# Performance work log

Hardware: AMD Instinct MI355X
Metric: run time of the kernel (lower is better)

Reference implementation:

```python
import jax, jax.numpy as jnp
import numpy as np

N = 10000        # nodes
E = 160000       # edges
H = 256          # hidden_dim
K = 20           # mixture components
NL = 5           # num_layers
NODE_F = 64      # node_feature_dim
NNT = 10         # num_node_types
NET = 5          # num_edge_types + 1


def setup_inputs() -> dict:
    key = jax.random.key(0)
    ks = iter(jax.random.split(key, 64))

    def nrm(shape, fan_in):
        return jax.random.normal(next(ks), shape, jnp.float32) * (1.0 / np.sqrt(fan_in))

    inp = {}
    inp["x"] = jax.random.normal(next(ks), (N, NODE_F), jnp.float32)
    inp["edge_attr"] = jax.random.normal(next(ks), (E,), jnp.float32)
    # embeddings (weights stored as [in, out])
    inp["neW"] = nrm((NODE_F, H), NODE_F); inp["neb"] = jnp.zeros((H,), jnp.float32)
    inp["eeW"] = nrm((1, H), 1);           inp["eeb"] = jnp.zeros((H,), jnp.float32)
    # per-layer message MLPs f, g (stacked over NL layers)
    inp["fW1"] = nrm((NL, 3 * H, H), 3 * H); inp["fb1"] = jnp.zeros((NL, H), jnp.float32)
    inp["fW2"] = nrm((NL, H, H), H);         inp["fb2"] = jnp.zeros((NL, H), jnp.float32)
    inp["gW1"] = nrm((NL, 3 * H, H), 3 * H); inp["gb1"] = jnp.zeros((NL, H), jnp.float32)
    inp["gW2"] = nrm((NL, H, H), H);         inp["gb2"] = jnp.zeros((NL, H), jnp.float32)
    # per-layer GRU (PyTorch layout: weight_ih [3H, 2H], weight_hh [3H, H], gate order r,z,n)
    inp["gru_wih"] = nrm((NL, 3 * H, 2 * H), 2 * H)
    inp["gru_whh"] = nrm((NL, 3 * H, H), H)
    inp["gru_bih"] = jnp.zeros((NL, 3 * H), jnp.float32)
    inp["gru_bhh"] = jnp.zeros((NL, 3 * H), jnp.float32)
    # mlp_alpha: 3H -> H -> K
    inp["aW1"] = nrm((3 * H, H), 3 * H); inp["ab1"] = jnp.zeros((H,), jnp.float32)
    inp["aW2"] = nrm((H, K), H);         inp["ab2"] = jnp.zeros((K,), jnp.float32)
    # node_pred: 2H -> H -> NNT
    inp["npW1"] = nrm((2 * H, H), 2 * H); inp["npb1"] = jnp.zeros((H,), jnp.float32)
    inp["npW2"] = nrm((H, NNT), H);       inp["npb2"] = jnp.zeros((NNT,), jnp.float32)
    # edge_pred: H -> H -> NET*K
    inp["epW1"] = nrm((H, H), H);          inp["epb1"] = jnp.zeros((H,), jnp.float32)
    inp["epW2"] = nrm((H, NET * K), H);    inp["epb2"] = jnp.zeros((NET * K,), jnp.float32)
    inp["edge_index"] = jax.random.randint(next(ks), (2, E), 0, N)
    inp["v_t"] = N - 1
    return inp


def reference(x, edge_attr, neW, neb, eeW, eeb,
              fW1, fb1, fW2, fb2, gW1, gb1, gW2, gb2,
              gru_wih, gru_whh, gru_bih, gru_bhh,
              aW1, ab1, aW2, ab2, npW1, npb1, npW2, npb2,
              epW1, epb1, epW2, epb2, edge_index, v_t):
    src = edge_index[0]  # x_j
    dst = edge_index[1]  # x_i (aggregation target)

    h_v = x @ neW + neb                       # [N, H]
    h_e = edge_attr[:, None] @ eeW + eeb      # [E, H]

    for l in range(NL):
        cat = jnp.concatenate([h_v[dst], h_v[src], h_e], axis=-1)   # [E, 3H]
        m = jax.nn.relu(cat @ fW1[l] + fb1[l]) @ fW2[l] + fb2[l]    # [E, H]
        a = jax.nn.relu(cat @ gW1[l] + gb1[l]) @ gW2[l] + gb2[l]    # [E, H]
        agg = jax.ops.segment_sum(m * a, dst, num_segments=N)       # [N, H]
        # nn.GRU over the node dimension as a sequence (unbatched input [N, 2H])
        gi = jnp.concatenate([h_v, agg], axis=-1) @ gru_wih[l].T + gru_bih[l]  # [N, 3H]
        whh, bhh = gru_whh[l], gru_bhh[l]

        def step(h, g):
            gh = whh @ h + bhh
            ir, iz, i_n = jnp.split(g, 3)
            hr, hz, hn = jnp.split(gh, 3)
            r = jax.nn.sigmoid(ir + hr)
            z = jax.nn.sigmoid(iz + hz)
            n = jnp.tanh(i_n + r * hn)
            h2 = (1.0 - z) * n + z * h
            return h2, h2

        _, h_v = jax.lax.scan(step, jnp.zeros((H,), h_v.dtype), gi)  # [N, H]

    ge = jnp.broadcast_to(jnp.mean(h_v, axis=0), h_v.shape)          # [N, H]
    np_in = jnp.concatenate([ge, h_v], axis=-1)                      # [N, 2H]
    node_pred = jax.nn.relu(np_in @ npW1 + npb1) @ npW2 + npb2       # [N, NNT]

    h_v_t = jnp.broadcast_to(h_v[v_t], h_v.shape)                    # [N, H]
    al_in = jnp.concatenate([ge, h_v_t, h_v], axis=-1)               # [N, 3H]
    alphas = jax.nn.relu(al_in @ aW1 + ab1) @ aW2 + ab2              # [N, K]
    alphas = jax.nn.softmax(jnp.sum(alphas, axis=0, keepdims=True), axis=1)  # [1, K]

    p_v = jax.nn.softmax(node_pred, axis=-1)
    log_theta = (jax.nn.relu(h_v @ epW1 + epb1) @ epW2 + epb2).reshape(N, NET, K)
    p_e = jnp.sum(alphas * jax.nn.softmax(log_theta, axis=1), axis=-1)  # [N, NET]
    return p_v, p_e
```

## Files before the change

### kernel.cpp

```cpp
#include <hip/hip_runtime.h>
#include <hip/hip_bf16.h>

#define NN 10000
#define NE 160000

typedef _Float16 half8 __attribute__((ext_vector_type(8)));
typedef _Float16 half2v __attribute__((ext_vector_type(2)));
typedef float f32x4 __attribute__((ext_vector_type(4)));

__device__ __forceinline__ f32x4 mfma_f16(half8 a, half8 b, f32x4 c){
  return __builtin_amdgcn_mfma_f32_16x16x32_f16(a, b, c, 0, 0, 0);
}

#if defined(__has_builtin)
#if __has_builtin(__builtin_amdgcn_fdot2)
#define HAS_FDOT2 1
#endif
#endif

__device__ __forceinline__ float fdot2f(half2v a, half2v b, float c){
#ifdef HAS_FDOT2
  return __builtin_amdgcn_fdot2(a, b, c, false);
#else
  return c + (float)a[0]*(float)b[0] + (float)a[1]*(float)b[1];
#endif
}

__global__ void zero_f32_kernel(float* __restrict__ p, int n){
  int i = blockIdx.x*blockDim.x + threadIdx.x;
  int st = gridDim.x*blockDim.x;
  for (; i < n; i += st) p[i] = 0.f;
}

__global__ void cast_f16_kernel(const float* __restrict__ a, _Float16* __restrict__ o, int n){
  int i = blockIdx.x*blockDim.x + threadIdx.x;
  int st = gridDim.x*blockDim.x;
  for (; i < n; i += st) o[i] = (_Float16)a[i];
}

__global__ void prep_w1t_kernel(const float* __restrict__ f, const float* __restrict__ g,
                                _Float16* __restrict__ fT, _Float16* __restrict__ gT){
  int i = blockIdx.x*256 + threadIdx.x;
  if (i >= 5*256*768) return;
  int l = i / (256*768); int r = i % (256*768);
  int c = r / 768; int k = r % 768;
  size_t s = (size_t)l*768*256 + (size_t)k*256 + c;
  fT[i] = (_Float16)f[s]; gT[i] = (_Float16)g[s];
}
__global__ void prep_w2t_kernel(const float* __restrict__ f, const float* __restrict__ g,
                                _Float16* __restrict__ fT, _Float16* __restrict__ gT){
  int i = blockIdx.x*256 + threadIdx.x;
  if (i >= 5*256*256) return;
  int l = i / (256*256); int r = i % (256*256);
  int c = r / 256; int k = r % 256;
  size_t s = (size_t)l*256*256 + (size_t)k*256 + c;
  fT[i] = (_Float16)f[s]; gT[i] = (_Float16)g[s];
}

__global__ void hist_kernel(const int* __restrict__ dst, int* __restrict__ cnt){
  int e = blockIdx.x*256 + threadIdx.x;
  if (e < NE) atomicAdd(&cnt[dst[e]], 1);
}

__global__ __launch_bounds__(1024) void scan_off_kernel(const int* __restrict__ cnt, int* __restrict__ cur){
  __shared__ int sA[1024];
  const int t = threadIdx.x;
  int run = 0;
  for (int ch = 0; ch < 10; ++ch){
    int idx = ch*1024 + t;
    int v = (idx < NN) ? cnt[idx] : 0;
    sA[t] = v;
    __syncthreads();
    for (int o = 1; o < 1024; o <<= 1){
      int add = (t >= o) ? sA[t-o] : 0;
      __syncthreads();
      sA[t] += add;
      __syncthreads();
    }
    if (idx < NN) cur[idx] = run + sA[t] - v;
    run += sA[1023];
    __syncthreads();
  }
}

__global__ void scatter_kernel(const int* __restrict__ eidx, const float* __restrict__ ea,
                               int* __restrict__ cur, int* __restrict__ srcS,
                               int* __restrict__ dstS, float* __restrict__ eaS){
  int e = blockIdx.x*256 + threadIdx.x;
  if (e < NE){
    int d = eidx[NE + e];
    int p = atomicAdd(&cur[d], 1);
    srcS[p] = eidx[e];
    dstS[p] = d;
    eaS[p]  = ea[e];
  }
}

__global__ __launch_bounds__(256) void embed_kernel(const float* __restrict__ x,
    const float* __restrict__ neW, const float* __restrict__ neb,
    float* __restrict__ hv, _Float16* __restrict__ hvf){
  __shared__ float sx[16*64];
  int rb = blockIdx.x*16, t = threadIdx.x;
  for (int i = t; i < 16*64; i += 256) sx[i] = x[(size_t)rb*64 + i];
  __syncthreads();
  float acc[16];
  float bb = neb[t];
  #pragma unroll
  for (int r = 0; r < 16; r++) acc[r] = bb;
  for (int c = 0; c < 64; c++){
    float w = neW[c*256 + t];
    #pragma unroll
    for (int r = 0; r < 16; r++) acc[r] += sx[r*64 + c]*w;
  }
  for (int r = 0; r < 16; r++){
    hv [(size_t)(rb+r)*256 + t] = acc[r];
    hvf[(size_t)(rb+r)*256 + t] = (_Float16)acc[r];
  }
}

__global__ __launch_bounds__(256, 2) void edge_mlp_kernel(
    const _Float16* __restrict__ hvf, const float* __restrict__ eaS,
    const int* __restrict__ srcS, const int* __restrict__ dstS,
    const float* __restrict__ eeW, const float* __restrict__ eeb,
    const _Float16* __restrict__ fW1T, const float* __restrict__ fb1,
    const _Float16* __restrict__ fW2T, const float* __restrict__ fb2,
    const _Float16* __restrict__ gW1T, const float* __restrict__ gb1,
    const _Float16* __restrict__ gW2T, const float* __restrict__ gb2,
    float* __restrict__ agg)
{
  extern __shared__ char smem[];
  _Float16* sHid = (_Float16*)smem;
  float* sProd = (float*)smem;
  float* sEW  = (float*)(smem + 64*264*2);
  float* sEB  = sEW + 256;
  int*   sDst = (int*)(sEB + 256);

  const int tid = threadIdx.x;
  const int wave = tid >> 6, lane = tid & 63;
  const int l15 = lane & 15, l4 = lane >> 4;
  const int eb = blockIdx.x*64;
  if (tid < 256){ sEW[tid] = eeW[tid]; sEB[tid] = eeb[tid]; }
  if (tid < 64)  sDst[tid] = dstS[eb + tid];
  int dd[4], ss[4]; float ea[4];
  #pragma unroll
  for (int rt = 0; rt < 4; rt++){
    int e = eb + rt*16 + l15;
    dd[rt] = dstS[e]; ss[rt] = srcS[e]; ea[rt] = eaS[e];
  }
  __syncthreads();
  const int colw = wave*64;
  const f32x4 zf = {0.f, 0.f, 0.f, 0.f};

  f32x4 accM[4][4], accA[4][4];
  #pragma unroll
  for (int a_ = 0; a_ < 4; a_++)
    #pragma unroll
    for (int b_ = 0; b_ < 4; b_++){ accM[a_][b_] = zf; accA[a_][b_] = zf; }

  {
    f32x4 acc[4][4];
    #pragma unroll
    for (int a_ = 0; a_ < 4; a_++)
      #pragma unroll
      for (int b_ = 0; b_ < 4; b_++) acc[a_][b_] = zf;
    #pragma unroll 1
    for (int kc = 0; kc < 24; ++kc){
      const int kk = kc*32 + l4*8;
      half8 aF[4];
      if (kc < 8){
        #pragma unroll
        for (int rt = 0; rt < 4; rt++) aF[rt] = *(const half8*)(hvf + (size_t)dd[rt]*256 + kk);
      } else if (kc < 16){
        #pragma unroll
        for (int rt = 0; rt < 4; rt++) aF[rt] = *(const half8*)(hvf + (size_t)ss[rt]*256 + (kk - 256));
      } else {
        const int q = kk - 512;
        #pragma unroll
        for (int rt = 0; rt < 4; rt++){
          half8 v;
          #pragma unroll
          for (int j = 0; j < 8; j++) v[j] = (_Float16)(ea[rt]*sEW[q+j] + sEB[q+j]);
          aF[rt] = v;
        }
      }
      half8 bF[4];
      #pragma unroll
      for (int ct = 0; ct < 4; ct++)
        bF[ct] = *(const half8*)(fW1T + (size_t)(colw + ct*16 + l15)*768 + kk);
      #pragma unroll
      for (int rt = 0; rt < 4; rt++)
        #pragma unroll
        for (int ct = 0; ct < 4; ct++)
          acc[rt][ct] = mfma_f16(aF[rt], bF[ct], acc[rt][ct]);
    }
    #pragma unroll
    for (int ct = 0; ct < 4; ct++){
      const int col = colw + ct*16 + l15;
      const float bb = fb1[col];
      #pragma unroll
      for (int rt = 0; rt < 4; rt++)
        #pragma unroll
        for (int ri = 0; ri < 4; ri++){
          int row = rt*16 + l4*4 + ri;
          sHid[row*264 + col] = (_Float16)fmaxf(acc[rt][ct][ri] + bb, 0.f);
        }
    }
    __syncthreads();
    #pragma unroll 1
    for (int kc = 0; kc < 8; ++kc){
      const int kk = kc*32 + l4*8;
      half8 aF[4], bF[4];
      #pragma unroll
      for (int rt = 0; rt < 4; rt++) aF[rt] = *(const half8*)(sHid + (rt*16 + l15)*264 + kk);
      #pragma unroll
      for (int ct = 0; ct < 4; ct++) bF[ct] = *(const half8*)(fW2T + (size_t)(colw + ct*16 + l15)*256 + kk);
      #pragma unroll
      for (int rt = 0; rt < 4; rt++)
        #pragma unroll
        for (int ct = 0; ct < 4; ct++)
          accM[rt][ct] = mfma_f16(aF[rt], bF[ct], accM[rt][ct]);
    }
    __syncthreads();
  }

  {
    f32x4 acc[4][4];
    #pragma unroll
    for (int a_ = 0; a_ < 4; a_++)
      #pragma unroll
      for (int b_ = 0; b_ < 4; b_++) acc[a_][b_] = zf;
    #pragma unroll 1
    for (int kc = 0; kc < 24; ++kc){
      const int kk = kc*32 + l4*8;
      half8 aF[4];
      if (kc < 8){
        #pragma unroll
        for (int rt = 0; rt < 4; rt++) aF[rt] = *(const half8*)(hvf + (size_t)dd[rt]*256 + kk);
      } else if (kc < 16){
        #pragma unroll
        for (int rt = 0; rt < 4; rt++) aF[rt] = *(const half8*)(hvf + (size_t)ss[rt]*256 + (kk - 256));
      } else {
        const int q = kk - 512;
        #pragma unroll
        for (int rt = 0; rt < 4; rt++){
          half8 v;
          #pragma unroll
          for (int j = 0; j < 8; j++) v[j] = (_Float16)(ea[rt]*sEW[q+j] + sEB[q+j]);
          aF[rt] = v;
        }
      }
      half8 bF[4];
      #pragma unroll
      for (int ct = 0; ct < 4; ct++)
        bF[ct] = *(const half8*)(gW1T + (size_t)(colw + ct*16 + l15)*768 + kk);
      #pragma unroll
      for (int rt = 0; rt < 4; rt++)
        #pragma unroll
        for (int ct = 0; ct < 4; ct++)
          acc[rt][ct] = mfma_f16(aF[rt], bF[ct], acc[rt][ct]);
    }
    #pragma unroll
    for (int ct = 0; ct < 4; ct++){
      const int col = colw + ct*16 + l15;
      const float bb = gb1[col];
      #pragma unroll
      for (int rt = 0; rt < 4; rt++)
        #pragma unroll
        for (int ri = 0; ri < 4; ri++){
          int row = rt*16 + l4*4 + ri;
          sHid[row*264 + col] = (_Float16)fmaxf(acc[rt][ct][ri] + bb, 0.f);
        }
    }
    __syncthreads();
    #pragma unroll 1
    for (int kc = 0; kc < 8; ++kc){
      const int kk = kc*32 + l4*8;
      half8 aF[4], bF[4];
      #pragma unroll
      for (int rt = 0; rt < 4; rt++) aF[rt] = *(const half8*)(sHid + (rt*16 + l15)*264 + kk);
      #pragma unroll
      for (int ct = 0; ct < 4; ct++) bF[ct] = *(const half8*)(gW2T + (size_t)(colw + ct*16 + l15)*256 + kk);
      #pragma unroll
      for (int rt = 0; rt < 4; rt++)
        #pragma unroll
        for (int ct = 0; ct < 4; ct++)
          accA[rt][ct] = mfma_f16(aF[rt], bF[ct], accA[rt][ct]);
    }
    __syncthreads();
  }

  int cd = sDst[0]; float ac = 0.f;
  #pragma unroll 1
  for (int hf = 0; hf < 2; ++hf){
    #pragma unroll
    for (int ct = 0; ct < 4; ct++){
      const int col = colw + ct*16 + l15;
      const float bm = fb2[col], ba = gb2[col];
      #pragma unroll
      for (int rt2 = 0; rt2 < 2; rt2++){
        const int rt = hf*2 + rt2;
        #pragma unroll
        for (int ri = 0; ri < 4; ri++){
          int row = rt2*16 + l4*4 + ri;
          sProd[row*264 + col] = (accM[rt][ct][ri] + bm)*(accA[rt][ct][ri] + ba);
        }
      }
    }
    __syncthreads();
    for (int r = 0; r < 32; ++r){
      float v = sProd[r*264 + tid];
      int dr = sDst[hf*32 + r];
      if (dr != cd){ atomicAdd(&agg[(size_t)cd*256 + tid], ac); ac = 0.f; cd = dr; }
      ac += v;
    }
    __syncthreads();
  }
  atomicAdd(&agg[(size_t)cd*256 + tid], ac);
}

#define RB_GI 157
__global__ __launch_bounds__(256, 3) void gi_mfma_kernel(
    const _Float16* __restrict__ hvf, const _Float16* __restrict__ aggf,
    const _Float16* __restrict__ wihL, const float* __restrict__ bihL,
    float* __restrict__ gi)
{
  const int tid = threadIdx.x;
  const int wave = tid >> 6, lane = tid & 63, l15 = lane & 15, l4 = lane >> 4;
  const int rblk = blockIdx.x % RB_GI;
  const int cg   = blockIdx.x / RB_GI;
  const int rb = rblk*64;
  const int colw = cg*256 + wave*64;
  int rowc[4];
  #pragma unroll
  for (int rt = 0; rt < 4; rt++){ int r = rb + rt*16 + l15; rowc[rt] = (r < NN) ? r : NN-1; }
  const f32x4 zf = {0.f, 0.f, 0.f, 0.f};
  f32x4 acc[4][4];
  #pragma unroll
  for (int a_ = 0; a_ < 4; a_++)
    #pragma unroll
    for (int b_ = 0; b_ < 4; b_++) acc[a_][b_] = zf;
  #pragma unroll 1
  for (int kc = 0; kc < 16; ++kc){
    const int kk = kc*32 + l4*8;
    half8 aF[4], bF[4];
    if (kc < 8){
      #pragma unroll
      for (int rt = 0; rt < 4; rt++) aF[rt] = *(const half8*)(hvf + (size_t)rowc[rt]*256 + kk);
    } else {
      #pragma unroll
      for (int rt = 0; rt < 4; rt++) aF[rt] = *(const half8*)(aggf + (size_t)rowc[rt]*256 + (kk - 256));
    }
    #pragma unroll
    for (int ct = 0; ct < 4; ct++)
      bF[ct] = *(const half8*)(wihL + (size_t)(colw + ct*16 + l15)*512 + kk);
    #pragma unroll
    for (int rt = 0; rt < 4; rt++)
      #pragma unroll
      for (int ct = 0; ct < 4; ct++)
        acc[rt][ct] = mfma_f16(aF[rt], bF[ct], acc[rt][ct]);
  }
  #pragma unroll
  for (int ct = 0; ct < 4; ct++){
    const int col = colw + ct*16 + l15;
    const float bb = bihL[col];
    #pragma unroll
    for (int rt = 0; rt < 4; rt++)
      #pragma unroll
      for (int ri = 0; ri < 4; ri++){
        int row = rb + rt*16 + l4*4 + ri;
        if (row < NN) gi[(size_t)row*768 + col] = acc[rt][ct][ri] + bb;
      }
  }
}

#define FOR32(M) M(0) M(1) M(2) M(3) M(4) M(5) M(6) M(7) M(8) M(9) M(10) M(11) M(12) M(13) M(14) M(15) \
                 M(16) M(17) M(18) M(19) M(20) M(21) M(22) M(23) M(24) M(25) M(26) M(27) M(28) M(29) M(30) M(31)

#define DECL_W(i) half8 w##i;

#define LD8(dst, q, i) { float4 _a = (q)[2*(i)], _b = (q)[2*(i)+1]; \
  dst[0]=(_Float16)_a.x; dst[1]=(_Float16)_a.y; dst[2]=(_Float16)_a.z; dst[3]=(_Float16)_a.w; \
  dst[4]=(_Float16)_b.x; dst[5]=(_Float16)_b.y; dst[6]=(_Float16)_b.z; dst[7]=(_Float16)_b.w; }

#define LOAD_W(i) LD8(w##i, q0, i)

#define DOT_STEP(i) { half8 hh = ph[i]; \
  a0 = fdot2f(__builtin_shufflevector(w##i, w##i, 0, 1), __builtin_shufflevector(hh, hh, 0, 1), a0); \
  a1 = fdot2f(__builtin_shufflevector(w##i, w##i, 2, 3), __builtin_shufflevector(hh, hh, 2, 3), a1); \
  a2 = fdot2f(__builtin_shufflevector(w##i, w##i, 4, 5), __builtin_shufflevector(hh, hh, 4, 5), a2); \
  a3 = fdot2f(__builtin_shufflevector(w##i, w##i, 6, 7), __builtin_shufflevector(hh, hh, 6, 7), a3); }

__global__ __launch_bounds__(768, 1) void gru_scan7(
    const float* __restrict__ whhL, const float* __restrict__ bhhL,
    const float* __restrict__ gi, float* __restrict__ hv, _Float16* __restrict__ hvf)
{
  const int t = threadIdx.x;
  FOR32(DECL_W)
  {
    const float4* q0 = (const float4*)(whhL + (size_t)t*256);
    FOR32(LOAD_W)
  }
  const float bh = bhhL[t];
  __shared__ float sGH[768];
  __shared__ __align__(16) _Float16 sH16[256];
  float h = 0.f;
  if (t < 256) sH16[t] = (_Float16)0.f;
  float gr = 0.f, gz = 0.f, gn = 0.f;
  if (t < 256){ gr = gi[t]; gz = gi[256 + t]; gn = gi[512 + t]; }
  __syncthreads();
  #pragma unroll 1
  for (int step = 0; step < NN; ++step){
    float pr = 0.f, pz = 0.f, pn = 0.f;
    if (t < 256){
      const float* g = gi + (size_t)((step + 1 < NN) ? step + 1 : step)*768;
      pr = g[t]; pz = g[256 + t]; pn = g[512 + t];
    }
    const half8* ph = (const half8*)sH16;
    float a0 = 0.f, a1 = 0.f, a2 = 0.f, a3 = 0.f;
    FOR32(DOT_STEP)
    sGH[t] = (a0 + a1) + (a2 + a3) + bh;
    __syncthreads();
    if (t < 256){
      float hr = sGH[t], hz = sGH[256 + t], hn = sGH[512 + t];
      float r = 1.f/(1.f + __expf(-(gr + hr)));
      float z = 1.f/(1.f + __expf(-(gz + hz)));
      float xx = gn + r*hn;
      xx = fminf(fmaxf(xx, -15.f), 15.f);
      float e2 = __expf(2.f*xx);
      float n = (e2 - 1.f)/(e2 + 1.f);
      h = n + z*(h - n);
      hv [(size_t)step*256 + t] = h;
      hvf[(size_t)step*256 + t] = (_Float16)h;
      sH16[t] = (_Float16)h;
      gr = pr; gz = pz; gn = pn;
    }
    __syncthreads();
  }
}

__global__ __launch_bounds__(256) void ge_sum_kernel(const float* __restrict__ hv, float* __restrict__ ge){
  int rb = blockIdx.x*40, t = threadIdx.x;
  float s = 0.f;
  for (int i = 0; i < 40; i++) s += hv[(size_t)(rb + i)*256 + t];
  atomicAdd(&ge[t], s);
}

__global__ void finalize_kernel(const float* __restrict__ ge, const float* __restrict__ hv,
                                const int* __restrict__ vt, float* __restrict__ gem, float* __restrict__ hvt){
  int t = threadIdx.x;
  gem[t] = ge[t]*(1.0f/NN);
  hvt[t] = hv[(size_t)vt[0]*256 + t];
}

__global__ __launch_bounds__(256) void base_np_kernel(const float* __restrict__ gem,
    const float* __restrict__ npW1, const float* __restrict__ npb1, float* __restrict__ bnp){
  __shared__ float sg[256];
  int t = threadIdx.x; sg[t] = gem[t]; __syncthreads();
  float a = npb1[t];
  for (int c = 0; c < 256; c++) a += sg[c]*npW1[c*256 + t];
  bnp[t] = a;
}

__global__ __launch_bounds__(256) void base_al_kernel(const float* __restrict__ gem,
    const float* __restrict__ hvt, const float* __restrict__ aW1,
    const float* __restrict__ ab1, float* __restrict__ bal){
  __shared__ float sg[256], sv[256];
  int t = threadIdx.x; sg[t] = gem[t]; sv[t] = hvt[t]; __syncthreads();
  float a = ab1[t];
  for (int c = 0; c < 256; c++) a += sg[c]*aW1[c*256 + t];
  for (int c = 0; c < 256; c++) a += sv[c]*aW1[(256 + c)*256 + t];
  bal[t] = a;
}

__global__ __launch_bounds__(256) void node_pred_kernel(const float* __restrict__ hv,
    const float* __restrict__ bnp, const float* __restrict__ npW1,
    const float* __restrict__ npW2, const float* __restrict__ npb2,
    float* __restrict__ outPV){
  __shared__ float sHv[16*256];
  __shared__ float sHid[16*257];
  __shared__ float sLg[16*10];
  int rb = blockIdx.x*16, t = threadIdx.x;
  for (int i = t; i < 4096; i += 256) sHv[i] = hv[(size_t)rb*256 + i];
  __syncthreads();
  float acc[16]; float b = bnp[t];
  #pragma unroll
  for (int r = 0; r < 16; r++) acc[r] = b;
  for (int c = 0; c < 256; c++){
    float w = npW1[(256 + c)*256 + t];
    #pragma unroll
    for (int r = 0; r < 16; r++) acc[r] += sHv[r*256 + c]*w;
  }
  for (int r = 0; r < 16; r++) sHid[r*257 + t] = fmaxf(acc[r], 0.f);
  __syncthreads();
  {
    int r = t >> 4, u = t & 15;
    if (u < 10){
      float a = npb2[u];
      for (int c = 0; c < 256; c++) a += sHid[r*257 + c]*npW2[c*10 + u];
      sLg[r*10 + u] = a;
    }
  }
  __syncthreads();
  if (t < 16){
    float mx = -1e30f;
    for (int u = 0; u < 10; u++) mx = fmaxf(mx, sLg[t*10 + u]);
    float s = 0.f, e[10];
    for (int u = 0; u < 10; u++){ e[u] = __expf(sLg[t*10 + u] - mx); s += e[u]; }
    float inv = 1.f/s;
    for (int u = 0; u < 10; u++) outPV[(size_t)(rb + t)*10 + u] = e[u]*inv;
  }
}

__global__ __launch_bounds__(256) void alphas_kernel(const float* __restrict__ hv,
    const float* __restrict__ bal, const float* __restrict__ aW1,
    const float* __restrict__ aW2, const float* __restrict__ ab2,
    float* __restrict__ alsum){
  __shared__ float sHv[16*256];
  __shared__ float sHid[16*257];
  __shared__ float sAv[16*20];
  int rb = blockIdx.x*16, t = threadIdx.x;
  for (int i = t; i < 4096; i += 256) sHv[i] = hv[(size_t)rb*256 + i];
  __syncthreads();
  float acc[16]; float b = bal[t];
  #pragma unroll
  for (int r = 0; r < 16; r++) acc[r] = b;
  for (int c = 0; c < 256; c++){
    float w = aW1[(512 + c)*256 + t];
    #pragma unroll
    for (int r = 0; r < 16; r++) acc[r] += sHv[r*256 + c]*w;
  }
  for (int r = 0; r < 16; r++) sHid[r*257 + t] = fmaxf(acc[r], 0.f);
  __syncthreads();
  {
    int r = t >> 4, k = t & 15;
    float a = ab2[k];
    for (int c = 0; c < 256; c++) a += sHid[r*257 + c]*aW2[c*20 + k];
    sAv[r*20 + k] = a;
    if (k < 4){
      int k2 = 16 + k;
      float a2 = ab2[k2];
      for (int c = 0; c < 256; c++) a2 += sHid[r*257 + c]*aW2[c*20 + k2];
      sAv[r*20 + k2] = a2;
    }
  }
  __syncthreads();
  if (t < 20){
    float s = 0.f;
    for (int rr = 0; rr < 16; rr++) s += sAv[rr*20 + t];
    atomicAdd(&alsum[t], s);
  }
}

__global__ void alpha_softmax_kernel(const float* __restrict__ alsum, float* __restrict__ alph){
  if (threadIdx.x == 0){
    float mx = -1e30f;
    for (int k = 0; k < 20; k++) mx = fmaxf(mx, alsum[k]);
    float s = 0.f, e[20];
    for (int k = 0; k < 20; k++){ e[k] = __expf(alsum[k] - mx); s += e[k]; }
    for (int k = 0; k < 20; k++) alph[k] = e[k]/s;
  }
}

__global__ __launch_bounds__(256) void edge_pred_kernel(const float* __restrict__ hv,
    const float* __restrict__ epW1, const float* __restrict__ epb1,
    const float* __restrict__ epW2, const float* __restrict__ epb2,
    const float* __restrict__ alph, float* __restrict__ outPE){
  __shared__ float sHv[16*256];
  __shared__ float sHid[16*257];
  __shared__ float sLT[16*100];
  __shared__ float sPE[16*5];
  __shared__ float sAl[20];
  int rb = blockIdx.x*16, t = threadIdx.x;
  for (int i = t; i < 4096; i += 256) sHv[i] = hv[(size_t)rb*256 + i];
  if (t < 20) sAl[t] = alph[t];
  if (t < 80) sPE[t] = 0.f;
  __syncthreads();
  float acc[16]; float b = epb1[t];
  #pragma unroll
  for (int r = 0; r < 16; r++) acc[r] = b;
  for (int c = 0; c < 256; c++){
    float w = epW1[c*256 + t];
    #pragma unroll
    for (int r = 0; r < 16; r++) acc[r] += sHv[r*256 + c]*w;
  }
  for (int r = 0; r < 16; r++) sHid[r*257 + t] = fmaxf(acc[r], 0.f);
  __syncthreads();
  for (int p = 0; p < 7; p++){
    int idx = p*256 + t;
    if (idx < 1600){
      int r = idx/100, j = idx%100;
      float a = epb2[j];
      for (int c = 0; c < 256; c++) a += sHid[r*257 + c]*epW2[c*100 + j];
      sLT[r*100 + j] = a;
    }
  }
  __syncthreads();
  {
    int r = t >> 4, k = t & 15;
    for (int pass = 0; pass < 2; ++pass){
      int kk = pass ? (16 + k) : k;
      if (pass && k >= 4) break;
      float lt[5];
      #pragma unroll
      for (int net = 0; net < 5; net++) lt[net] = sLT[r*100 + net*20 + kk];
      float mx = lt[0];
      #pragma unroll
      for (int net = 1; net < 5; net++) mx = fmaxf(mx, lt[net]);
      float e[5], s = 0.f;
      #pragma unroll
      for (int net = 0; net < 5; net++){ e[net] = __expf(lt[net] - mx); s += e[net]; }
      float wgt = sAl[kk]/s;
      #pragma unroll
      for (int net = 0; net < 5; net++) atomicAdd(&sPE[r*5 + net], e[net]*wgt);
    }
  }
  __syncthreads();
  if (t < 80){
    int r = t/5, net = t%5;
    outPE[(size_t)(rb + r)*5 + net] = sPE[t];
  }
}

extern "C" void kernel_launch(void* const* d_in, const int* in_sizes, int n_in,
                              void* d_out, int out_size, void* d_ws, size_t ws_size,
                              hipStream_t stream){
  const float* x    = (const float*)d_in[0];
  const float* edge_attr = (const float*)d_in[1];
  const float* neW  = (const float*)d_in[2];
  const float* neb  = (const float*)d_in[3];
  const float* eeW  = (const float*)d_in[4];
  const float* eeb  = (const float*)d_in[5];
  const float* fW1  = (const float*)d_in[6];
  const float* fb1  = (const float*)d_in[7];
  const float* fW2  = (const float*)d_in[8];
  const float* fb2  = (const float*)d_in[9];
  const float* gW1  = (const float*)d_in[10];
  const float* gb1  = (const float*)d_in[11];
  const float* gW2  = (const float*)d_in[12];
  const float* gb2  = (const float*)d_in[13];
  const float* wih  = (const float*)d_in[14];
  const float* whh  = (const float*)d_in[15];
  const float* bih  = (const float*)d_in[16];
  const float* bhh  = (const float*)d_in[17];
  const float* aW1  = (const float*)d_in[18];
  const float* ab1  = (const float*)d_in[19];
  const float* aW2  = (const float*)d_in[20];
  const float* ab2  = (const float*)d_in[21];
  const float* npW1 = (const float*)d_in[22];
  const float* npb1 = (const float*)d_in[23];
  const float* npW2 = (const float*)d_in[24];
  const float* npb2 = (const float*)d_in[25];
  const float* epW1 = (const float*)d_in[26];
  const float* epb1 = (const float*)d_in[27];
  const float* epW2 = (const float*)d_in[28];
  const float* epb2 = (const float*)d_in[29];
  const int*   eidx = (const int*)d_in[30];
  const int*   vt   = (const int*)d_in[31];

  char* ws = (char*)d_ws;
  size_t off_ = 0;
  auto alloc = [&](size_t b){ size_t r = off_; off_ += (b + 511) & ~(size_t)511; return r; };
  float*    hv    = (float*)   (ws + alloc((size_t)NN*256*4));
  _Float16* hvf   = (_Float16*)(ws + alloc((size_t)NN*256*2));
  float*    agg   = (float*)   (ws + alloc((size_t)NN*256*4));
  _Float16* aggf  = (_Float16*)(ws + alloc((size_t)NN*256*2));
  float*    gi    = (float*)   (ws + alloc((size_t)NN*768*4));
  _Float16* fW1T  = (_Float16*)(ws + alloc((size_t)5*256*768*2));
  _Float16* gW1T  = (_Float16*)(ws + alloc((size_t)5*256*768*2));
  _Float16* fW2T  = (_Float16*)(ws + alloc((size_t)5*256*256*2));
  _Float16* gW2T  = (_Float16*)(ws + alloc((size_t)5*256*256*2));
  _Float16* wihf  = (_Float16*)(ws + alloc((size_t)5*768*512*2));
  int*      cnt   = (int*)     (ws + alloc((size_t)NN*4));
  int*      cur   = (int*)     (ws + alloc((size_t)NN*4));
  int*      srcS  = (int*)     (ws + alloc((size_t)NE*4));
  int*      dstS  = (int*)     (ws + alloc((size_t)NE*4));
  float*    eaS   = (float*)   (ws + alloc((size_t)NE*4));
  float*    ge    = (float*)   (ws + alloc(256*4));
  float*    gem   = (float*)   (ws + alloc(256*4));
  float*    hvt   = (float*)   (ws + alloc(256*4));
  float*    bnp   = (float*)   (ws + alloc(256*4));
  float*    bal   = (float*)   (ws + alloc(256*4));
  float*    alsum = (float*)   (ws + alloc(128));
  float*    alph  = (float*)   (ws + alloc(128));

  float* outPV = (float*)d_out;
  float* outPE = outPV + (size_t)NN*10;

  prep_w1t_kernel<<<3840, 256, 0, stream>>>(fW1, gW1, fW1T, gW1T);
  prep_w2t_kernel<<<1280, 256, 0, stream>>>(fW2, gW2, fW2T, gW2T);
  cast_f16_kernel<<<2048, 256, 0, stream>>>(wih, wihf, 5*768*512);

  zero_f32_kernel<<<40, 256, 0, stream>>>((float*)cnt, NN);
  hist_kernel<<<625, 256, 0, stream>>>(eidx + NE, cnt);
  scan_off_kernel<<<1, 1024, 0, stream>>>(cnt, cur);
  scatter_kernel<<<625, 256, 0, stream>>>(eidx, edge_attr, cur, srcS, dstS, eaS);

  embed_kernel<<<625, 256, 0, stream>>>(x, neW, neb, hv, hvf);

  const size_t edge_lds = (size_t)64*264*2 + 2048 + 256;
  for (int l = 0; l < 5; ++l){
    zero_f32_kernel<<<2048, 256, 0, stream>>>(agg, NN*256);
    edge_mlp_kernel<<<2500, 256, edge_lds, stream>>>(hvf, eaS, srcS, dstS, eeW, eeb,
        fW1T + (size_t)l*256*768, fb1 + l*256, fW2T + (size_t)l*256*256, fb2 + l*256,
        gW1T + (size_t)l*256*768, gb1 + l*256, gW2T + (size_t)l*256*256, gb2 + l*256, agg);
    cast_f16_kernel<<<2048, 256, 0, stream>>>(agg, aggf, NN*256);
    gi_mfma_kernel<<<471, 256, 0, stream>>>(hvf, aggf, wihf + (size_t)l*768*512, bih + l*768, gi);
    gru_scan7<<<1, 768, 0, stream>>>(whh + (size_t)l*768*256, bhh + l*768, gi, hv, hvf);
  }

  zero_f32_kernel<<<1, 256, 0, stream>>>(ge, 256);
  zero_f32_kernel<<<1, 64, 0, stream>>>(alsum, 32);
  ge_sum_kernel<<<250, 256, 0, stream>>>(hv, ge);
  finalize_kernel<<<1, 256, 0, stream>>>(ge, hv, vt, gem, hvt);
  base_np_kernel<<<1, 256, 0, stream>>>(gem, npW1, npb1, bnp);
  base_al_kernel<<<1, 256, 0, stream>>>(gem, hvt, aW1, ab1, bal);
  node_pred_kernel<<<625, 256, 0, stream>>>(hv, bnp, npW1, npW2, npb2, outPV);
  alphas_kernel<<<625, 256, 0, stream>>>(hv, bal, aW1, aW2, ab2, alsum);
  alpha_softmax_kernel<<<1, 64, 0, stream>>>(alsum, alph);
  edge_pred_kernel<<<625, 256, 0, stream>>>(hv, epW1, epb1, epW2, epb2, alph, outPE);
}
```

Baseline: 64.81 ms.

## Restructure GRU scan to 256 threads each computing all three gates

The sequential GRU recurrence kernel now runs 256 threads instead of 768. Each thread holds the r, z and n rows of W_hh in registers, 96 half8 values, and computes all three gate dot products itself. This drops the shared-memory gate exchange and one of the two barriers per step; a double-buffered hidden-state array makes a single barrier enough. The cost is three times the per-thread dot-product work with fewer waves to hide latency, plus heavy register pressure that could cause spills.

```diff
diff --git a/kernel.cpp b/kernel.cpp
--- a/kernel.cpp
+++ b/kernel.cpp
@@ -376,64 +376,68 @@
 #define FOR32(M) M(0) M(1) M(2) M(3) M(4) M(5) M(6) M(7) M(8) M(9) M(10) M(11) M(12) M(13) M(14) M(15) \
                  M(16) M(17) M(18) M(19) M(20) M(21) M(22) M(23) M(24) M(25) M(26) M(27) M(28) M(29) M(30) M(31)
 
-#define DECL_W(i) half8 w##i;
+#define DECL_W3(i) half8 wr##i, wz##i, wn##i;
 
 #define LD8(dst, q, i) { float4 _a = (q)[2*(i)], _b = (q)[2*(i)+1]; \
   dst[0]=(_Float16)_a.x; dst[1]=(_Float16)_a.y; dst[2]=(_Float16)_a.z; dst[3]=(_Float16)_a.w; \
   dst[4]=(_Float16)_b.x; dst[5]=(_Float16)_b.y; dst[6]=(_Float16)_b.z; dst[7]=(_Float16)_b.w; }
 
-#define LOAD_W(i) LD8(w##i, q0, i)
-
-#define DOT_STEP(i) { half8 hh = ph[i]; \
-  a0 = fdot2f(__builtin_shufflevector(w##i, w##i, 0, 1), __builtin_shufflevector(hh, hh, 0, 1), a0); \
-  a1 = fdot2f(__builtin_shufflevector(w##i, w##i, 2, 3), __builtin_shufflevector(hh, hh, 2, 3), a1); \
-  a2 = fdot2f(__builtin_shufflevector(w##i, w##i, 4, 5), __builtin_shufflevector(hh, hh, 4, 5), a2); \
-  a3 = fdot2f(__builtin_shufflevector(w##i, w##i, 6, 7), __builtin_shufflevector(hh, hh, 6, 7), a3); }
-
-__global__ __launch_bounds__(768, 1) void gru_scan7(
+#define LOAD_W3(i) LD8(wr##i, q0, i) LD8(wz##i, q1, i) LD8(wn##i, q2, i)
+
+#define OPQ(i) asm volatile("" : "+v"(wr##i), "+v"(wz##i), "+v"(wn##i));
+
+#define SV(w, a, b) __builtin_shufflevector(w, w, a, b)
+
+#define DOT3(i) { half8 hh = ph[i]; \
+  half2v h0 = SV(hh, 0, 1), h1 = SV(hh, 2, 3), h2 = SV(hh, 4, 5), h3 = SV(hh, 6, 7); \
+  ar0 = fdot2f(SV(wr##i, 0, 1), h0, ar0); ar1 = fdot2f(SV(wr##i, 2, 3), h1, ar1); \
+  ar0 = fdot2f(SV(wr##i, 4, 5), h2, ar0); ar1 = fdot2f(SV(wr##i, 6, 7), h3, ar1); \
+  az0 = fdot2f(SV(wz##i, 0, 1), h0, az0); az1 = fdot2f(SV(wz##i, 2, 3), h1, az1); \
+  az0 = fdot2f(SV(wz##i, 4, 5), h2, az0); az1 = fdot2f(SV(wz##i, 6, 7), h3, az1); \
+  an0 = fdot2f(SV(wn##i, 0, 1), h0, an0); an1 = fdot2f(SV(wn##i, 2, 3), h1, an1); \
+  an0 = fdot2f(SV(wn##i, 4, 5), h2, an0); an1 = fdot2f(SV(wn##i, 6, 7), h3, an1); }
+
+__global__ __attribute__((amdgpu_flat_work_group_size(256, 256), amdgpu_waves_per_eu(1, 1)))
+void gru_scan8(
     const float* __restrict__ whhL, const float* __restrict__ bhhL,
     const float* __restrict__ gi, float* __restrict__ hv, _Float16* __restrict__ hvf)
 {
   const int t = threadIdx.x;
-  FOR32(DECL_W)
+  FOR32(DECL_W3)
   {
     const float4* q0 = (const float4*)(whhL + (size_t)t*256);
-    FOR32(LOAD_W)
-  }
-  const float bh = bhhL[t];
-  __shared__ float sGH[768];
-  __shared__ __align__(16) _Float16 sH16[256];
+    const float4* q1 = (const float4*)(whhL + (size_t)(256 + t)*256);
+    const float4* q2 = (const float4*)(whhL + (size_t)(512 + t)*256);
+    FOR32(LOAD_W3)
+  }
+  FOR32(OPQ)
+  const float br = bhhL[t], bz = bhhL[256 + t], bn = bhhL[512 + t];
+  __shared__ __align__(16) _Float16 sH16[2][256];
   float h = 0.f;
-  if (t < 256) sH16[t] = (_Float16)0.f;
-  float gr = 0.f, gz = 0.f, gn = 0.f;
-  if (t < 256){ gr = gi[t]; gz = gi[256 + t]; gn = gi[512 + t]; }
+  sH16[0][t] = (_Float16)0.f;
+  float gr = gi[t], gz = gi[256 + t], gn = gi[512 + t];
   __syncthreads();
   #pragma unroll 1
   for (int step = 0; step < NN; ++step){
-    float pr = 0.f, pz = 0.f, pn = 0.f;
-    if (t < 256){
-      const float* g = gi + (size_t)((step + 1 < NN) ? step + 1 : step)*768;
-      pr = g[t]; pz = g[256 + t]; pn = g[512 + t];
-    }
-    const half8* ph = (const half8*)sH16;
-    float a0 = 0.f, a1 = 0.f, a2 = 0.f, a3 = 0.f;
-    FOR32(DOT_STEP)
-    sGH[t] = (a0 + a1) + (a2 + a3) + bh;
-    __syncthreads();
-    if (t < 256){
-      float hr = sGH[t], hz = sGH[256 + t], hn = sGH[512 + t];
-      float r = 1.f/(1.f + __expf(-(gr + hr)));
-      float z = 1.f/(1.f + __expf(-(gz + hz)));
-      float xx = gn + r*hn;
-      xx = fminf(fmaxf(xx, -15.f), 15.f);
-      float e2 = __expf(2.f*xx);
-      float n = (e2 - 1.f)/(e2 + 1.f);
-      h = n + z*(h - n);
-      hv [(size_t)step*256 + t] = h;
-      hvf[(size_t)step*256 + t] = (_Float16)h;
-      sH16[t] = (_Float16)h;
-      gr = pr; gz = pz; gn = pn;
-    }
+    const float* g = gi + (size_t)((step + 1 < NN) ? step + 1 : step)*768;
+    float pr = g[t], pz = g[256 + t], pn = g[512 + t];
+    const half8* ph = (const half8*)sH16[step & 1];
+    float ar0 = 0.f, ar1 = 0.f, az0 = 0.f, az1 = 0.f, an0 = 0.f, an1 = 0.f;
+    FOR32(DOT3)
+    float hr = ar0 + ar1 + br;
+    float hz = az0 + az1 + bz;
+    float hn = an0 + an1 + bn;
+    float r = 1.f/(1.f + __expf(-(gr + hr)));
+    float z = 1.f/(1.f + __expf(-(gz + hz)));
+    float xx = gn + r*hn;
+    xx = fminf(fmaxf(xx, -15.f), 15.f);
+    float e2 = __expf(2.f*xx);
+    float n = (e2 - 1.f)/(e2 + 1.f);
+    h = n + z*(h - n);
+    hv [(size_t)step*256 + t] = h;
+    hvf[(size_t)step*256 + t] = (_Float16)h;
+    sH16[(step + 1) & 1][t] = (_Float16)h;
+    gr = pr; gz = pz; gn = pn;
     __syncthreads();
   }
 }
@@ -705,7 +709,7 @@
         gW1T + (size_t)l*256*768, gb1 + l*256, gW2T + (size_t)l*256*256, gb2 + l*256, agg);
     cast_f16_kernel<<<2048, 256, 0, stream>>>(agg, aggf, NN*256);
     gi_mfma_kernel<<<471, 256, 0, stream>>>(hvf, aggf, wihf + (size_t)l*768*512, bih + l*768, gi);
-    gru_scan7<<<1, 768, 0, stream>>>(whh + (size_t)l*768*256, bhh + l*768, gi, hv, hvf);
+    gru_scan8<<<1, 256, 0, stream>>>(whh + (size_t)l*768*256, bhh + l*768, gi, hv, hvf);
   }
 
   zero_f32_kernel<<<1, 256, 0, stream>>>(ge, 256);
```

After: 104.5 ms. +61.2%, slower.

## Compute GRU hidden-state matvec with MFMA and AGPR-resident weights in the scan

Applied to the files above, without the earlier changes.

Replaces the per-thread fdot2 recurrent matvec in the sequential GRU scan with 16x16x32 f16 MFMA instructions. Eight waves each hold a 96-row slice of W_hh in AGPRs, and the hidden vector is broadcast as the B operand; only column 0 of each output tile is written to shared memory. The hidden state in LDS is now double-buffered, and the hh bias add moves into the gate stage. The block drops from 768 to 512 threads. Because every B column is the same vector, 15/16 of the MFMA work is redundant, and the cost is traded against fewer LDS reads and shorter per-step dependency chains.

```diff
diff --git a/kernel.cpp b/kernel.cpp
--- a/kernel.cpp
+++ b/kernel.cpp
@@ -10,20 +10,6 @@
 
 __device__ __forceinline__ f32x4 mfma_f16(half8 a, half8 b, f32x4 c){
   return __builtin_amdgcn_mfma_f32_16x16x32_f16(a, b, c, 0, 0, 0);
-}
-
-#if defined(__has_builtin)
-#if __has_builtin(__builtin_amdgcn_fdot2)
-#define HAS_FDOT2 1
-#endif
-#endif
-
-__device__ __forceinline__ float fdot2f(half2v a, half2v b, float c){
-#ifdef HAS_FDOT2
-  return __builtin_amdgcn_fdot2(a, b, c, false);
-#else
-  return c + (float)a[0]*(float)b[0] + (float)a[1]*(float)b[1];
-#endif
 }
 
 __global__ void zero_f32_kernel(float* __restrict__ p, int n){
@@ -373,41 +359,55 @@
   }
 }
 
-#define FOR32(M) M(0) M(1) M(2) M(3) M(4) M(5) M(6) M(7) M(8) M(9) M(10) M(11) M(12) M(13) M(14) M(15) \
-                 M(16) M(17) M(18) M(19) M(20) M(21) M(22) M(23) M(24) M(25) M(26) M(27) M(28) M(29) M(30) M(31)
-
-#define DECL_W(i) half8 w##i;
-
-#define LD8(dst, q, i) { float4 _a = (q)[2*(i)], _b = (q)[2*(i)+1]; \
-  dst[0]=(_Float16)_a.x; dst[1]=(_Float16)_a.y; dst[2]=(_Float16)_a.z; dst[3]=(_Float16)_a.w; \
-  dst[4]=(_Float16)_b.x; dst[5]=(_Float16)_b.y; dst[6]=(_Float16)_b.z; dst[7]=(_Float16)_b.w; }
-
-#define LOAD_W(i) LD8(w##i, q0, i)
-
-#define DOT_STEP(i) { half8 hh = ph[i]; \
-  a0 = fdot2f(__builtin_shufflevector(w##i, w##i, 0, 1), __builtin_shufflevector(hh, hh, 0, 1), a0); \
-  a1 = fdot2f(__builtin_shufflevector(w##i, w##i, 2, 3), __builtin_shufflevector(hh, hh, 2, 3), a1); \
-  a2 = fdot2f(__builtin_shufflevector(w##i, w##i, 4, 5), __builtin_shufflevector(hh, hh, 4, 5), a2); \
-  a3 = fdot2f(__builtin_shufflevector(w##i, w##i, 6, 7), __builtin_shufflevector(hh, hh, 6, 7), a3); }
-
-__global__ __launch_bounds__(768, 1) void gru_scan7(
+#define FOR6(M) M(0) M(1) M(2) M(3) M(4) M(5)
+#define FOR8K(M) M(0) M(1) M(2) M(3) M(4) M(5) M(6) M(7)
+
+__device__ __forceinline__ half8 ld8f(const float* p){
+  float4 x = *(const float4*)p;
+  float4 y = *(const float4*)(p + 4);
+  half8 d;
+  d[0]=(_Float16)x.x; d[1]=(_Float16)x.y; d[2]=(_Float16)x.z; d[3]=(_Float16)x.w;
+  d[4]=(_Float16)y.x; d[5]=(_Float16)y.y; d[6]=(_Float16)y.z; d[7]=(_Float16)y.w;
+  return d;
+}
+
+#define DECL_A(tr) half8 A##tr##_0, A##tr##_1, A##tr##_2, A##tr##_3, A##tr##_4, A##tr##_5, A##tr##_6, A##tr##_7;
+
+#define LOAD_A(tr) { const float* wr = whhL + (size_t)(w*96 + tr*16 + l15)*256 + l4*8; \
+  A##tr##_0 = ld8f(wr);       A##tr##_1 = ld8f(wr + 32);  A##tr##_2 = ld8f(wr + 64);  A##tr##_3 = ld8f(wr + 96); \
+  A##tr##_4 = ld8f(wr + 128); A##tr##_5 = ld8f(wr + 160); A##tr##_6 = ld8f(wr + 192); A##tr##_7 = ld8f(wr + 224); }
+
+#define PIN_A(tr) asm volatile("" : "+a"(A##tr##_0), "+a"(A##tr##_1), "+a"(A##tr##_2), "+a"(A##tr##_3), \
+                                    "+a"(A##tr##_4), "+a"(A##tr##_5), "+a"(A##tr##_6), "+a"(A##tr##_7));
+
+#define MFMA_KT(kt) { half8 b = *(const half8*)(hbuf + kt*32 + l4*8); \
+  d0 = mfma_f16(A0_##kt, b, d0); d1 = mfma_f16(A1_##kt, b, d1); d2 = mfma_f16(A2_##kt, b, d2); \
+  d3 = mfma_f16(A3_##kt, b, d3); d4 = mfma_f16(A4_##kt, b, d4); d5 = mfma_f16(A5_##kt, b, d5); }
+
+#define EXT_D(tr) { sGH[rbase + tr*16 + 0] = d##tr[0]; sGH[rbase + tr*16 + 1] = d##tr[1]; \
+                    sGH[rbase + tr*16 + 2] = d##tr[2]; sGH[rbase + tr*16 + 3] = d##tr[3]; }
+
+__global__ __launch_bounds__(512, 1) void gru_scan10(
     const float* __restrict__ whhL, const float* __restrict__ bhhL,
     const float* __restrict__ gi, float* __restrict__ hv, _Float16* __restrict__ hvf)
 {
   const int t = threadIdx.x;
-  FOR32(DECL_W)
-  {
-    const float4* q0 = (const float4*)(whhL + (size_t)t*256);
-    FOR32(LOAD_W)
-  }
-  const float bh = bhhL[t];
+  const int w = t >> 6;
+  const int lane = t & 63;
+  const int l15 = lane & 15, l4 = lane >> 4;
+  FOR6(DECL_A)
+  FOR6(LOAD_A)
+  FOR6(PIN_A)
+  float br = 0.f, bz = 0.f, bn = 0.f;
+  if (t < 256){ br = bhhL[t]; bz = bhhL[256 + t]; bn = bhhL[512 + t]; }
+  __shared__ __align__(16) _Float16 sH16[2][256];
   __shared__ float sGH[768];
-  __shared__ __align__(16) _Float16 sH16[256];
   float h = 0.f;
-  if (t < 256) sH16[t] = (_Float16)0.f;
+  if (t < 256) sH16[0][t] = (_Float16)0.f;
   float gr = 0.f, gz = 0.f, gn = 0.f;
   if (t < 256){ gr = gi[t]; gz = gi[256 + t]; gn = gi[512 + t]; }
   __syncthreads();
+  const f32x4 zf = {0.f, 0.f, 0.f, 0.f};
   #pragma unroll 1
   for (int step = 0; step < NN; ++step){
     float pr = 0.f, pz = 0.f, pn = 0.f;
@@ -415,13 +415,18 @@
       const float* g = gi + (size_t)((step + 1 < NN) ? step + 1 : step)*768;
       pr = g[t]; pz = g[256 + t]; pn = g[512 + t];
     }
-    const half8* ph = (const half8*)sH16;
-    float a0 = 0.f, a1 = 0.f, a2 = 0.f, a3 = 0.f;
-    FOR32(DOT_STEP)
-    sGH[t] = (a0 + a1) + (a2 + a3) + bh;
+    const _Float16* hbuf = sH16[step & 1];
+    f32x4 d0 = zf, d1 = zf, d2 = zf, d3 = zf, d4 = zf, d5 = zf;
+    FOR8K(MFMA_KT)
+    if (l15 == 0){
+      const int rbase = w*96 + l4*4;
+      FOR6(EXT_D)
+    }
     __syncthreads();
     if (t < 256){
-      float hr = sGH[t], hz = sGH[256 + t], hn = sGH[512 + t];
+      float hr = sGH[t] + br;
+      float hz = sGH[256 + t] + bz;
+      float hn = sGH[512 + t] + bn;
       float r = 1.f/(1.f + __expf(-(gr + hr)));
       float z = 1.f/(1.f + __expf(-(gz + hz)));
       float xx = gn + r*hn;
@@ -431,7 +436,7 @@
       h = n + z*(h - n);
       hv [(size_t)step*256 + t] = h;
       hvf[(size_t)step*256 + t] = (_Float16)h;
-      sH16[t] = (_Float16)h;
+      sH16[(step + 1) & 1][t] = (_Float16)h;
       gr = pr; gz = pz; gn = pn;
     }
     __syncthreads();
@@ -705,7 +710,7 @@
         gW1T + (size_t)l*256*768, gb1 + l*256, gW2T + (size_t)l*256*256, gb2 + l*256, agg);
     cast_f16_kernel<<<2048, 256, 0, stream>>>(agg, aggf, NN*256);
     gi_mfma_kernel<<<471, 256, 0, stream>>>(hvf, aggf, wihf + (size_t)l*768*512, bih + l*768, gi);
-    gru_scan7<<<1, 768, 0, stream>>>(whh + (size_t)l*768*256, bhh + l*768, gi, hv, hvf);
+    gru_scan10<<<1, 512, 0, stream>>>(whh + (size_t)l*768*256, bhh + l*768, gi, hv, hvf);
   }
 
   zero_f32_kernel<<<1, 256, 0, stream>>>(ge, 256);
```

After: 66.62 ms. 1.03x slower.

## Stream packed fp16 GRU hidden weights from L2 each step instead of registers

Applied to the files above, without the earlier changes.

The GRU scan kernel no longer keeps its 256 hidden-weight fp16 values in registers for all steps. Instead a prep kernel packs W_hh into a coalesced [chunk][thread][8] fp16 layout, and every step re-loads the weights from global memory with double-buffered prefetching. This frees about 128 VGPRs per thread, cutting register pressure and possible spilling at 768 threads. The cost is 384KB of weight traffic per step across 10000 serial steps, which depends on cache hit latency being hidden.

```diff
diff --git a/kernel.cpp b/kernel.cpp
--- a/kernel.cpp
+++ b/kernel.cpp
@@ -55,6 +55,17 @@
   int c = r / 256; int k = r % 256;
   size_t s = (size_t)l*256*256 + (size_t)k*256 + c;
   fT[i] = (_Float16)f[s]; gT[i] = (_Float16)g[s];
+}
+
+__global__ void prep_whhPk_kernel(const float* __restrict__ whh, _Float16* __restrict__ pk){
+  int idx = blockIdx.x*256 + threadIdx.x;
+  if (idx >= 5*32*768) return;
+  int l = idx / (32*768); int r = idx % (32*768);
+  int i = r / 768; int t = r % 768;
+  const float* s = whh + (size_t)l*768*256 + (size_t)t*256 + i*8;
+  _Float16* d = pk + (size_t)idx*8;
+  #pragma unroll
+  for (int e = 0; e < 8; e++) d[e] = (_Float16)s[e];
 }
 
 __global__ void hist_kernel(const int* __restrict__ dst, int* __restrict__ cnt){
@@ -373,33 +384,25 @@
   }
 }
 
-#define FOR32(M) M(0) M(1) M(2) M(3) M(4) M(5) M(6) M(7) M(8) M(9) M(10) M(11) M(12) M(13) M(14) M(15) \
-                 M(16) M(17) M(18) M(19) M(20) M(21) M(22) M(23) M(24) M(25) M(26) M(27) M(28) M(29) M(30) M(31)
-
-#define DECL_W(i) half8 w##i;
-
-#define LD8(dst, q, i) { float4 _a = (q)[2*(i)], _b = (q)[2*(i)+1]; \
-  dst[0]=(_Float16)_a.x; dst[1]=(_Float16)_a.y; dst[2]=(_Float16)_a.z; dst[3]=(_Float16)_a.w; \
-  dst[4]=(_Float16)_b.x; dst[5]=(_Float16)_b.y; dst[6]=(_Float16)_b.z; dst[7]=(_Float16)_b.w; }
-
-#define LOAD_W(i) LD8(w##i, q0, i)
-
-#define DOT_STEP(i) { half8 hh = ph[i]; \
-  a0 = fdot2f(__builtin_shufflevector(w##i, w##i, 0, 1), __builtin_shufflevector(hh, hh, 0, 1), a0); \
-  a1 = fdot2f(__builtin_shufflevector(w##i, w##i, 2, 3), __builtin_shufflevector(hh, hh, 2, 3), a1); \
-  a2 = fdot2f(__builtin_shufflevector(w##i, w##i, 4, 5), __builtin_shufflevector(hh, hh, 4, 5), a2); \
-  a3 = fdot2f(__builtin_shufflevector(w##i, w##i, 6, 7), __builtin_shufflevector(hh, hh, 6, 7), a3); }
-
-__global__ __launch_bounds__(768, 1) void gru_scan7(
-    const float* __restrict__ whhL, const float* __restrict__ bhhL,
+#define SVv(w, a, b) __builtin_shufflevector(w, w, a, b)
+
+#define DOT8(w, h, acc) { \
+  acc = fdot2f(SVv(w,0,1), SVv(h,0,1), acc); acc = fdot2f(SVv(w,2,3), SVv(h,2,3), acc); \
+  acc = fdot2f(SVv(w,4,5), SVv(h,4,5), acc); acc = fdot2f(SVv(w,6,7), SVv(h,6,7), acc); }
+
+#define LDPK(i) (*(const half8*)(pk + ((size_t)(i)*768 + t)*8))
+
+#define PHASE(p, C0, C1, C2, C3, N0, N1, N2, N3) { \
+  if ((p) < 7){ N0 = LDPK(4*(p)+4); N1 = LDPK(4*(p)+5); N2 = LDPK(4*(p)+6); N3 = LDPK(4*(p)+7); } \
+  half8 h0 = ph[4*(p)+0], h1 = ph[4*(p)+1], h2 = ph[4*(p)+2], h3 = ph[4*(p)+3]; \
+  DOT8(C0, h0, a0) DOT8(C1, h1, a1) DOT8(C2, h2, a2) DOT8(C3, h3, a3) }
+
+__global__ __launch_bounds__(768, 1) void gru_scan12(
+    const _Float16* __restrict__ pk,
+    const float* __restrict__ bhhL,
     const float* __restrict__ gi, float* __restrict__ hv, _Float16* __restrict__ hvf)
 {
   const int t = threadIdx.x;
-  FOR32(DECL_W)
-  {
-    const float4* q0 = (const float4*)(whhL + (size_t)t*256);
-    FOR32(LOAD_W)
-  }
   const float bh = bhhL[t];
   __shared__ float sGH[768];
   __shared__ __align__(16) _Float16 sH16[256];
@@ -417,7 +420,16 @@
     }
     const half8* ph = (const half8*)sH16;
     float a0 = 0.f, a1 = 0.f, a2 = 0.f, a3 = 0.f;
-    FOR32(DOT_STEP)
+    half8 Wa0 = LDPK(0), Wa1 = LDPK(1), Wa2 = LDPK(2), Wa3 = LDPK(3);
+    half8 Wb0, Wb1, Wb2, Wb3;
+    PHASE(0, Wa0, Wa1, Wa2, Wa3, Wb0, Wb1, Wb2, Wb3)
+    PHASE(1, Wb0, Wb1, Wb2, Wb3, Wa0, Wa1, Wa2, Wa3)
+    PHASE(2, Wa0, Wa1, Wa2, Wa3, Wb0, Wb1, Wb2, Wb3)
+    PHASE(3, Wb0, Wb1, Wb2, Wb3, Wa0, Wa1, Wa2, Wa3)
+    PHASE(4, Wa0, Wa1, Wa2, Wa3, Wb0, Wb1, Wb2, Wb3)
+    PHASE(5, Wb0, Wb1, Wb2, Wb3, Wa0, Wa1, Wa2, Wa3)
+    PHASE(6, Wa0, Wa1, Wa2, Wa3, Wb0, Wb1, Wb2, Wb3)
+    PHASE(7, Wb0, Wb1, Wb2, Wb3, Wa0, Wa1, Wa2, Wa3)
     sGH[t] = (a0 + a1) + (a2 + a3) + bh;
     __syncthreads();
     if (t < 256){
@@ -670,6 +682,7 @@
   _Float16* fW2T  = (_Float16*)(ws + alloc((size_t)5*256*256*2));
   _Float16* gW2T  = (_Float16*)(ws + alloc((size_t)5*256*256*2));
   _Float16* wihf  = (_Float16*)(ws + alloc((size_t)5*768*512*2));
+  _Float16* whhPk = (_Float16*)(ws + alloc((size_t)5*32*768*8*2));
   int*      cnt   = (int*)     (ws + alloc((size_t)NN*4));
   int*      cur   = (int*)     (ws + alloc((size_t)NN*4));
   int*      srcS  = (int*)     (ws + alloc((size_t)NE*4));
@@ -689,6 +702,7 @@
   prep_w1t_kernel<<<3840, 256, 0, stream>>>(fW1, gW1, fW1T, gW1T);
   prep_w2t_kernel<<<1280, 256, 0, stream>>>(fW2, gW2, fW2T, gW2T);
   cast_f16_kernel<<<2048, 256, 0, stream>>>(wih, wihf, 5*768*512);
+  prep_whhPk_kernel<<<480, 256, 0, stream>>>(whh, whhPk);
 
   zero_f32_kernel<<<40, 256, 0, stream>>>((float*)cnt, NN);
   hist_kernel<<<625, 256, 0, stream>>>(eidx + NE, cnt);
@@ -705,7 +719,7 @@
         gW1T + (size_t)l*256*768, gb1 + l*256, gW2T + (size_t)l*256*256, gb2 + l*256, agg);
     cast_f16_kernel<<<2048, 256, 0, stream>>>(agg, aggf, NN*256);
     gi_mfma_kernel<<<471, 256, 0, stream>>>(hvf, aggf, wihf + (size_t)l*768*512, bih + l*768, gi);
-    gru_scan7<<<1, 768, 0, stream>>>(whh + (size_t)l*768*256, bhh + l*768, gi, hv, hvf);
+    gru_scan12<<<1, 768, 0, stream>>>(whhPk + (size_t)l*32*768*8, bhh + l*768, gi, hv, hvf);
   }
 
   zero_f32_kernel<<<1, 256, 0, stream>>>(ge, 256);
```

Measured after the change: 62.45 ms. 1.04x faster.
